# Performance work log

Hardware: AMD Instinct MI355X
Metric: run time of the kernel (lower is better)

## Reference

```python
import jax, jax.numpy as jnp
import numpy as np

B, C, H = 8, 768, 12
TH = TW = 16
SH = SW = 32
N = TH * TW + SH * SW  # 1280


def setup_inputs() -> dict:
    key = jax.random.key(0)
    k1, k2, k3 = jax.random.split(key, 3)
    return {
        "x": jax.random.normal(k1, (B, N, C), jnp.float32),
        "qkv_w": jax.random.normal(k2, (3 * C, C), jnp.float32) * 0.02,
        "proj_w": jax.random.normal(k3, (C, C), jnp.float32) * 0.02,
        "proj_b": jnp.zeros((C,), jnp.float32),
        "t_h": TH, "t_w": TW, "s_h": SH, "s_w": SW,
    }


def reference(x, qkv_w, proj_w, proj_b, t_h, t_w, s_h, s_w):
    Bb, Nn, Cc = x.shape
    hd = Cc // H
    scale = hd ** -0.5
    nt = t_h * t_w
    ns = s_h * s_w
    # qkv projection: torch Linear computes x @ W.T
    qkv = (x @ qkv_w.T).reshape(Bb, Nn, 3, H, hd).transpose(2, 0, 3, 1, 4)
    q, k, v = qkv[0], qkv[1], qkv[2]  # each [B, H, N, hd]
    q_mt, q_s = q[:, :, :nt], q[:, :, nt:]
    k_mt, v_mt = k[:, :, :nt], v[:, :, :nt]
    # template queries attend only to template keys
    attn_t = jax.nn.softmax(jnp.einsum('bhqd,bhkd->bhqk', q_mt, k_mt) * scale, axis=-1)
    x_mt = jnp.einsum('bhqk,bhkd->bhqd', attn_t, v_mt).transpose(0, 2, 1, 3).reshape(Bb, nt, Cc)
    # search queries attend to all (template + search) keys
    attn_s = jax.nn.softmax(jnp.einsum('bhqd,bhkd->bhqk', q_s, k) * scale, axis=-1)
    x_s = jnp.einsum('bhqk,bhkd->bhqd', attn_s, v).transpose(0, 2, 1, 3).reshape(Bb, ns, Cc)
    out = jnp.concatenate([x_mt, x_s], axis=1)
    out = out @ proj_w.T + proj_b
    return out
```

## Files before the change

kernel.cpp:

```cpp
#include <hip/hip_runtime.h>
#include <hip/hip_bf16.h>


typedef __attribute__((ext_vector_type(8))) short s8v;
typedef __attribute__((ext_vector_type(4))) float f4v;
typedef __attribute__((ext_vector_type(4))) unsigned short u4v;
typedef __attribute__((ext_vector_type(4))) unsigned int u4i;
typedef __attribute__((ext_vector_type(2))) unsigned int u2i;

#define MFMA16(a, b, c) __builtin_amdgcn_mfma_f32_16x16x32_bf16((a), (b), (c), 0, 0, 0)

#define QSCALE 0.1803368801f

__device__ __forceinline__ unsigned short f2bf(float f) {
  unsigned int u = __builtin_bit_cast(unsigned int, f);
  u += 0x7fffu + ((u >> 16) & 1u);
  return (unsigned short)(u >> 16);
}

__device__ __forceinline__ unsigned int pk2(float lo, float hi) {
  __hip_bfloat162 t = __float22bfloat162_rn(make_float2(lo, hi));
  unsigned int u;
  __builtin_memcpy(&u, &t, 4);
  return u;
}

__device__ __forceinline__ s8v pack8(const float* p0, const float* p1) {
  u4i pi;
  pi[0] = pk2(p0[0], p0[1]);
  pi[1] = pk2(p0[2], p0[3]);
  pi[2] = pk2(p1[0], p1[1]);
  pi[3] = pk2(p1[2], p1[3]);
  return __builtin_bit_cast(s8v, pi);
}

__global__ __launch_bounds__(256) void cvt3_kernel(const float* __restrict__ x,
                                                   const float* __restrict__ wq,
                                                   const float* __restrict__ wp,
                                                   unsigned short* __restrict__ xb,
                                                   unsigned short* __restrict__ wqb,
                                                   unsigned short* __restrict__ wpb) {
  int i = blockIdx.x * 256 + threadIdx.x;
  const float* src;
  unsigned short* dst;
  int j;
  if (i < 1966080) {
    src = x; dst = xb; j = i;
  } else if (i < 1966080 + 442368) {
    src = wq; dst = wqb; j = i - 1966080;
  } else {
    src = wp; dst = wpb; j = i - (1966080 + 442368);
  }
  f4v v = ((const f4v*)src)[j];
  u4v o;
  o[0] = f2bf(v[0]); o[1] = f2bf(v[1]); o[2] = f2bf(v[2]); o[3] = f2bf(v[3]);
  ((u4v*)dst)[j] = o;
}


#define GEMM_STAGE(AS, BS, kt_)                                                             \
  do {                                                                                      \
    __builtin_amdgcn_global_load_lds(                                                       \
        (const __attribute__((address_space(1))) unsigned int*)(gA0 + (kt_)),               \
        (__attribute__((address_space(3))) unsigned int*)((char*)(AS) + tid * 16), 16, 0, 0); \
    __builtin_amdgcn_global_load_lds(                                                       \
        (const __attribute__((address_space(1))) unsigned int*)(gB0 + (kt_)),               \
        (__attribute__((address_space(3))) unsigned int*)((char*)(BS) + tid * 16), 16, 0, 0); \
    __builtin_amdgcn_global_load_lds(                                                       \
        (const __attribute__((address_space(1))) unsigned int*)(gA1 + (kt_)),               \
        (__attribute__((address_space(3))) unsigned int*)((char*)(AS) + (256 + tid) * 16),  \
        16, 0, 0);                                                                          \
    __builtin_amdgcn_global_load_lds(                                                       \
        (const __attribute__((address_space(1))) unsigned int*)(gB1 + (kt_)),               \
        (__attribute__((address_space(3))) unsigned int*)((char*)(BS) + (256 + tid) * 16),  \
        16, 0, 0);                                                                          \
  } while (0)

__global__ __launch_bounds__(256) void gemm_qkv_kernel(
    const unsigned short* __restrict__ A,
    const unsigned short* __restrict__ Bm,
    unsigned short* __restrict__ qb, unsigned short* __restrict__ kb,
    unsigned short* __restrict__ vT) {
  const int K = 768;
  __shared__ __align__(16) unsigned short As[2][128 * 32];
  __shared__ __align__(16) unsigned short Bs[2][128 * 32];
  int tid = threadIdx.x;
  int wave = tid >> 6, lane = tid & 63;
  int quad = lane >> 4, l16 = lane & 15;
  int wm = wave >> 1, wn = wave & 1;
  int m0 = blockIdx.y * 128, n0 = blockIdx.x * 128;

  int srow = tid >> 2, scol = (tid & 3) << 3;
  const unsigned short* gA0 = A + (size_t)(m0 + srow) * K + scol;
  const unsigned short* gA1 = A + (size_t)(m0 + srow + 64) * K + scol;
  const unsigned short* gB0 = Bm + (size_t)(n0 + srow) * K + scol;
  const unsigned short* gB1 = Bm + (size_t)(n0 + srow + 64) * K + scol;

  f4v acc[4][4];
#pragma unroll
  for (int i = 0; i < 4; ++i)
#pragma unroll
    for (int j = 0; j < 4; ++j) acc[i][j] = (f4v){0.f, 0.f, 0.f, 0.f};

  GEMM_STAGE(As[0], Bs[0], 0);

  for (int t = 0; t < 24; ++t) {
    __syncthreads();
    int bf = t & 1;
    if (t + 1 < 24) GEMM_STAGE(As[bf ^ 1], Bs[bf ^ 1], (t + 1) * 32);

    const unsigned short* Ab = As[bf];
    const unsigned short* Bb = Bs[bf];
    s8v af[4], bfr[4];
#pragma unroll
    for (int mi = 0; mi < 4; ++mi)
      af[mi] = *(const s8v*)&Ab[(wm * 64 + mi * 16 + l16) * 32 + quad * 8];
#pragma unroll
    for (int ni = 0; ni < 4; ++ni)
      bfr[ni] = *(const s8v*)&Bb[(wn * 64 + ni * 16 + l16) * 32 + quad * 8];
#pragma unroll
    for (int mi = 0; mi < 4; ++mi)
#pragma unroll
      for (int ni = 0; ni < 4; ++ni)
        acc[mi][ni] = MFMA16(af[mi], bfr[ni], acc[mi][ni]);
  }

  int which = n0 / 768;
  if (which == 2) {
#pragma unroll
    for (int ni = 0; ni < 4; ++ni) {
      int oo = n0 + wn * 64 + ni * 16 + l16 - 1536;
      int hh = oo >> 6;
      int dd = oo & 63;
#pragma unroll
      for (int mi = 0; mi < 4; ++mi) {
        int gm = m0 + wm * 64 + mi * 16 + quad * 4;
        int bb = gm / 1280;
        int nn = gm - bb * 1280;
        u2i w;
        w[0] = pk2(acc[mi][ni][0], acc[mi][ni][1]);
        w[1] = pk2(acc[mi][ni][2], acc[mi][ni][3]);
        *(u2i*)(vT + (((size_t)bb * 12 + hh) * 64 + dd) * 1280 + nn) = w;
      }
    }
  } else {
    unsigned short* dst = which ? kb : qb;
    float sc = which ? 1.0f : QSCALE;
#pragma unroll
    for (int ni = 0; ni < 4; ++ni) {
      int oo = n0 + wn * 64 + ni * 16 + l16 - which * 768;
      int hh = oo >> 6;
      int dd = oo & 63;
#pragma unroll
      for (int mi = 0; mi < 4; ++mi) {
#pragma unroll
        for (int r = 0; r < 4; ++r) {
          int gm = m0 + wm * 64 + mi * 16 + quad * 4 + r;
          int bb = gm / 1280;
          int nn = gm - bb * 1280;
          dst[(((size_t)bb * 12 + hh) * 1280 + nn) * 64 + dd] = f2bf(acc[mi][ni][r] * sc);
        }
      }
    }
  }
}

__global__ __launch_bounds__(256) void gemm_proj_kernel(
    const unsigned short* __restrict__ A,
    const unsigned short* __restrict__ Bm,
    const float* __restrict__ pb, float* __restrict__ out) {
  const int K = 768;
  __shared__ __align__(16) unsigned short As[2][128 * 32];
  __shared__ __align__(16) unsigned short Bs[2][128 * 32];
  int tid = threadIdx.x;
  int wave = tid >> 6, lane = tid & 63;
  int quad = lane >> 4, l16 = lane & 15;
  int wm = wave >> 1, wn = wave & 1;
  int m0 = blockIdx.y * 128, n0 = blockIdx.x * 128;

  int srow = tid >> 2, scol = (tid & 3) << 3;
  const unsigned short* gA0 = A + (size_t)(m0 + srow) * K + scol;
  const unsigned short* gA1 = A + (size_t)(m0 + srow + 64) * K + scol;
  const unsigned short* gB0 = Bm + (size_t)(n0 + srow) * K + scol;
  const unsigned short* gB1 = Bm + (size_t)(n0 + srow + 64) * K + scol;

  f4v acc[4][4];
#pragma unroll
  for (int i = 0; i < 4; ++i)
#pragma unroll
    for (int j = 0; j < 4; ++j) acc[i][j] = (f4v){0.f, 0.f, 0.f, 0.f};

  GEMM_STAGE(As[0], Bs[0], 0);

  for (int t = 0; t < 24; ++t) {
    __syncthreads();
    int bf = t & 1;
    if (t + 1 < 24) GEMM_STAGE(As[bf ^ 1], Bs[bf ^ 1], (t + 1) * 32);

    const unsigned short* Ab = As[bf];
    const unsigned short* Bb = Bs[bf];
    s8v af[4], bfr[4];
#pragma unroll
    for (int mi = 0; mi < 4; ++mi)
      af[mi] = *(const s8v*)&Ab[(wm * 64 + mi * 16 + l16) * 32 + quad * 8];
#pragma unroll
    for (int ni = 0; ni < 4; ++ni)
      bfr[ni] = *(const s8v*)&Bb[(wn * 64 + ni * 16 + l16) * 32 + quad * 8];
#pragma unroll
    for (int mi = 0; mi < 4; ++mi)
#pragma unroll
      for (int ni = 0; ni < 4; ++ni)
        acc[mi][ni] = MFMA16(af[mi], bfr[ni], acc[mi][ni]);
  }

#pragma unroll
  for (int ni = 0; ni < 4; ++ni) {
    int gn = n0 + wn * 64 + ni * 16 + l16;
    float bias = pb[gn];
#pragma unroll
    for (int mi = 0; mi < 4; ++mi)
#pragma unroll
      for (int r = 0; r < 4; ++r) {
        int gm = m0 + wm * 64 + mi * 16 + quad * 4 + r;
        out[(size_t)gm * 768 + gn] = acc[mi][ni][r] + bias;
      }
  }
}

__global__ __launch_bounds__(256) void attn_kernel(
    const unsigned short* __restrict__ qb, const unsigned short* __restrict__ kb,
    const unsigned short* __restrict__ vT, unsigned short* __restrict__ attnb) {
  const int NT = 1280, CC = 768;
  int bx = blockIdx.x;
  int h = blockIdx.y;
  int b = blockIdx.z;
  int nk, qstart;
  if (bx < 8) { nk = 1280; qstart = 256 + bx * 128; }
  else        { nk = 256;  qstart = (bx - 8) * 128; }
  int wave = threadIdx.x >> 6, lane = threadIdx.x & 63;
  int quad = lane >> 4, l16 = lane & 15;
  int qa = qstart + wave * 32;
  int ntiles = nk >> 6;

  const unsigned short* qp = qb + (((size_t)b * 12 + h) * NT + qa) * 64;
  const unsigned short* kp = kb + (((size_t)b * 12 + h) * NT) * 64;
  const unsigned short* vp = vT + (((size_t)b * 12 + h) * 64) * NT;

  __shared__ __align__(16) unsigned short Kl[2][8][512];
  __shared__ __align__(16) unsigned short Vl[2][8][512];

  s8v bq0 = *(const s8v*)(qp + l16 * 64 + quad * 8);
  s8v bq1 = *(const s8v*)(qp + l16 * 64 + 32 + quad * 8);
  s8v bq2 = *(const s8v*)(qp + (16 + l16) * 64 + quad * 8);
  s8v bq3 = *(const s8v*)(qp + (16 + l16) * 64 + 32 + quad * 8);

  int perm = ((l16 >> 2) << 3) + (l16 & 3);
  int f0 = wave * 2, f1 = wave * 2 + 1;
  int koffs0, koffs1, voffs0, voffs1;
  {
    int s = f0 >> 2, dh = (f0 >> 1) & 1, hh = f0 & 1;
    koffs0 = (s * 32 + hh * 4 + perm) * 64 + (dh * 4 + quad) * 8;
    s = f1 >> 2; dh = (f1 >> 1) & 1; hh = f1 & 1;
    koffs1 = (s * 32 + hh * 4 + perm) * 64 + (dh * 4 + quad) * 8;
    int dt = f0 >> 1, sv = f0 & 1;
    voffs0 = (dt * 16 + l16) * NT + sv * 32 + quad * 8;
    dt = f1 >> 1; sv = f1 & 1;
    voffs1 = (dt * 16 + l16) * NT + sv * 32 + quad * 8;
  }

#define STAGE(bfi, k0_)                                                                     \
  do {                                                                                      \
    __builtin_amdgcn_global_load_lds(                                                       \
        (const __attribute__((address_space(1))) unsigned int*)(kp + (size_t)(k0_)*64 +     \
                                                                koffs0),                    \
        (__attribute__((address_space(3))) unsigned int*)((char*)&Kl[bfi][f0][0] +          \
                                                          lane * 16),                       \
        16, 0, 0);                                                                          \
    __builtin_amdgcn_global_load_lds(                                                       \
        (const __attribute__((address_space(1))) unsigned int*)(kp + (size_t)(k0_)*64 +     \
                                                                koffs1),                    \
        (__attribute__((address_space(3))) unsigned int*)((char*)&Kl[bfi][f1][0] +          \
                                                          lane * 16),                       \
        16, 0, 0);                                                                          \
    __builtin_amdgcn_global_load_lds(                                                       \
        (const __attribute__((address_space(1))) unsigned int*)(vp + (size_t)(k0_) +        \
                                                                voffs0),                    \
        (__attribute__((address_space(3))) unsigned int*)((char*)&Vl[bfi][f0][0] +          \
                                                          lane * 16),                       \
        16, 0, 0);                                                                          \
    __builtin_amdgcn_global_load_lds(                                                       \
        (const __attribute__((address_space(1))) unsigned int*)(vp + (size_t)(k0_) +        \
                                                                voffs1),                    \
        (__attribute__((address_space(3))) unsigned int*)((char*)&Vl[bfi][f1][0] +          \
                                                          lane * 16),                       \
        16, 0, 0);                                                                          \
  } while (0)

  float la = 0.f, lb = 0.f;
  f4v Oa[4], Ob[4];
#pragma unroll
  for (int dt = 0; dt < 4; ++dt) {
    Oa[dt] = (f4v){0.f, 0.f, 0.f, 0.f};
    Ob[dt] = (f4v){0.f, 0.f, 0.f, 0.f};
  }

  STAGE(0, 0);

  for (int t = 0; t < ntiles; ++t) {
    __syncthreads();
    int bf = t & 1;
    if (t + 1 < ntiles) STAGE(bf ^ 1, (t + 1) * 64);

    s8v kf[8], vf[8];
#pragma unroll
    for (int f = 0; f < 8; ++f) kf[f] = *(const s8v*)&Kl[bf][f][lane * 8];
#pragma unroll
    for (int g = 0; g < 8; ++g) vf[g] = *(const s8v*)&Vl[bf][g][lane * 8];

#pragma unroll
    for (int s = 0; s < 2; ++s) {
      int s4 = s << 2;
      f4v s0a = {0.f, 0.f, 0.f, 0.f}, s1a = {0.f, 0.f, 0.f, 0.f};
      f4v s0b = {0.f, 0.f, 0.f, 0.f}, s1b = {0.f, 0.f, 0.f, 0.f};
      s0a = MFMA16(kf[s4 | 0], bq0, s0a);
      s0a = MFMA16(kf[s4 | 2], bq1, s0a);
      s1a = MFMA16(kf[s4 | 1], bq0, s1a);
      s1a = MFMA16(kf[s4 | 3], bq1, s1a);
      s0b = MFMA16(kf[s4 | 0], bq2, s0b);
      s0b = MFMA16(kf[s4 | 2], bq3, s0b);
      s1b = MFMA16(kf[s4 | 1], bq2, s1b);
      s1b = MFMA16(kf[s4 | 3], bq3, s1b);

      float p0a[4], p1a[4], p0b[4], p1b[4];
#pragma unroll
      for (int r = 0; r < 4; ++r) {
        p0a[r] = __builtin_amdgcn_exp2f(s0a[r]);
        p1a[r] = __builtin_amdgcn_exp2f(s1a[r]);
        p0b[r] = __builtin_amdgcn_exp2f(s0b[r]);
        p1b[r] = __builtin_amdgcn_exp2f(s1b[r]);
      }
      la += ((p0a[0] + p0a[1]) + (p0a[2] + p0a[3])) + ((p1a[0] + p1a[1]) + (p1a[2] + p1a[3]));
      lb += ((p0b[0] + p0b[1]) + (p0b[2] + p0b[3])) + ((p1b[0] + p1b[1]) + (p1b[2] + p1b[3]));

      s8v pa = pack8(p0a, p1a);
      s8v pbv = pack8(p0b, p1b);

#pragma unroll
      for (int dt = 0; dt < 4; ++dt) {
        Oa[dt] = MFMA16(vf[dt * 2 + s], pa, Oa[dt]);
        Ob[dt] = MFMA16(vf[dt * 2 + s], pbv, Ob[dt]);
      }
    }
  }
#undef STAGE

  la += __shfl_xor(la, 16, 64);
  la += __shfl_xor(la, 32, 64);
  lb += __shfl_xor(lb, 16, 64);
  lb += __shfl_xor(lb, 32, 64);
  float inva = 1.f / la, invb = 1.f / lb;

  size_t rowa = ((size_t)b * NT + qa + l16) * CC + h * 64;
  size_t rowb = ((size_t)b * NT + qa + 16 + l16) * CC + h * 64;
#pragma unroll
  for (int dt = 0; dt < 4; ++dt) {
    u4v ova, ovb;
#pragma unroll
    for (int r = 0; r < 4; ++r) {
      ova[r] = f2bf(Oa[dt][r] * inva);
      ovb[r] = f2bf(Ob[dt][r] * invb);
    }
    *(u4v*)(attnb + rowa + dt * 16 + quad * 4) = ova;
    *(u4v*)(attnb + rowb + dt * 16 + quad * 4) = ovb;
  }
}

extern "C" void kernel_launch(void* const* d_in, const int* in_sizes, int n_in,
                              void* d_out, int out_size, void* d_ws, size_t ws_size,
                              hipStream_t stream) {
  const float* x = (const float*)d_in[0];
  const float* qkv_w = (const float*)d_in[1];
  const float* proj_w = (const float*)d_in[2];
  const float* proj_b = (const float*)d_in[3];
  float* out = (float*)d_out;

  char* ws = (char*)d_ws;
  unsigned short* xb = (unsigned short*)(ws + 0);
  unsigned short* wqkvb = (unsigned short*)(ws + 15728640);
  unsigned short* wpb = (unsigned short*)(ws + 19267584);
  unsigned short* qb = (unsigned short*)(ws + 20447232);
  unsigned short* kbuf = (unsigned short*)(ws + 36175872);
  unsigned short* vT = (unsigned short*)(ws + 51904512);
  unsigned short* attnb = xb;

  cvt3_kernel<<<dim3(9984), 256, 0, stream>>>(x, qkv_w, proj_w, xb, wqkvb, wpb);

  gemm_qkv_kernel<<<dim3(18, 80), 256, 0, stream>>>(xb, wqkvb, qb, kbuf, vT);
  attn_kernel<<<dim3(10, 12, 8), 256, 0, stream>>>(qb, kbuf, vT, attnb);
  gemm_proj_kernel<<<dim3(6, 80), 256, 0, stream>>>(attnb, wpb, proj_b, out);
}
```

Measured before the change: 272.0 us.

## Triple-buffer LDS loads with vmcnt waits and remap blocks per XCD

All three GEMM/attention kernels move from double to triple buffering in LDS. Two tiles are kept in flight, and each step waits with explicit s_waitcnt vmcnt(4) plus a raw s_barrier instead of __syncthreads. The grids are also flattened to 1D and remapped so consecutive blocks on the same XCD share rows or batch-heads, aiming for better L2 locality. The extra buffer raises LDS use, which may reduce occupancy. The hand-counted vmcnt value depends on each stage issuing exactly four loads per thread, which holds for the GEMMs but is less certain for the attention STAGE.

Result: faster. 242.0 us (-11.0%).

```diff
diff --git a/kernel.cpp b/kernel.cpp
--- a/kernel.cpp
+++ b/kernel.cpp
@@ -76,19 +76,32 @@
         16, 0, 0);                                                                          \
   } while (0)
 
+#define PIPE_WAIT(cond_more)                                                                \
+  do {                                                                                      \
+    if (cond_more) asm volatile("s_waitcnt vmcnt(4) lgkmcnt(0)" ::: "memory");              \
+    else           asm volatile("s_waitcnt vmcnt(0) lgkmcnt(0)" ::: "memory");              \
+    __builtin_amdgcn_s_barrier();                                                           \
+    __builtin_amdgcn_sched_barrier(0);                                                      \
+  } while (0)
+
 __global__ __launch_bounds__(256) void gemm_qkv_kernel(
     const unsigned short* __restrict__ A,
     const unsigned short* __restrict__ Bm,
     unsigned short* __restrict__ qb, unsigned short* __restrict__ kb,
     unsigned short* __restrict__ vT) {
   const int K = 768;
-  __shared__ __align__(16) unsigned short As[2][128 * 32];
-  __shared__ __align__(16) unsigned short Bs[2][128 * 32];
+  __shared__ __align__(16) unsigned short As[3][128 * 32];
+  __shared__ __align__(16) unsigned short Bs[3][128 * 32];
   int tid = threadIdx.x;
   int wave = tid >> 6, lane = tid & 63;
   int quad = lane >> 4, l16 = lane & 15;
   int wm = wave >> 1, wn = wave & 1;
-  int m0 = blockIdx.y * 128, n0 = blockIdx.x * 128;
+  int l = blockIdx.x;
+  int xcd = l & 7;
+  int idx = l >> 3;
+  int by = xcd * 10 + idx / 18;
+  int bxg = idx - (idx / 18) * 18;
+  int m0 = by * 128, n0 = bxg * 128;
 
   int srow = tid >> 2, scol = (tid & 3) << 3;
   const unsigned short* gA0 = A + (size_t)(m0 + srow) * K + scol;
@@ -103,14 +116,15 @@
     for (int j = 0; j < 4; ++j) acc[i][j] = (f4v){0.f, 0.f, 0.f, 0.f};
 
   GEMM_STAGE(As[0], Bs[0], 0);
-
+  GEMM_STAGE(As[1], Bs[1], 32);
+
+  int bfc = 0, bfs = 2;
   for (int t = 0; t < 24; ++t) {
-    __syncthreads();
-    int bf = t & 1;
-    if (t + 1 < 24) GEMM_STAGE(As[bf ^ 1], Bs[bf ^ 1], (t + 1) * 32);
-
-    const unsigned short* Ab = As[bf];
-    const unsigned short* Bb = Bs[bf];
+    PIPE_WAIT(t + 1 < 24);
+    if (t + 2 < 24) GEMM_STAGE(As[bfs], Bs[bfs], (t + 2) * 32);
+
+    const unsigned short* Ab = As[bfc];
+    const unsigned short* Bb = Bs[bfc];
     s8v af[4], bfr[4];
 #pragma unroll
     for (int mi = 0; mi < 4; ++mi)
@@ -123,6 +137,9 @@
 #pragma unroll
       for (int ni = 0; ni < 4; ++ni)
         acc[mi][ni] = MFMA16(af[mi], bfr[ni], acc[mi][ni]);
+
+    bfc = (bfc == 2) ? 0 : bfc + 1;
+    bfs = (bfs == 2) ? 0 : bfs + 1;
   }
 
   int which = n0 / 768;
@@ -170,13 +187,18 @@
     const unsigned short* __restrict__ Bm,
     const float* __restrict__ pb, float* __restrict__ out) {
   const int K = 768;
-  __shared__ __align__(16) unsigned short As[2][128 * 32];
-  __shared__ __align__(16) unsigned short Bs[2][128 * 32];
+  __shared__ __align__(16) unsigned short As[3][128 * 32];
+  __shared__ __align__(16) unsigned short Bs[3][128 * 32];
   int tid = threadIdx.x;
   int wave = tid >> 6, lane = tid & 63;
   int quad = lane >> 4, l16 = lane & 15;
   int wm = wave >> 1, wn = wave & 1;
-  int m0 = blockIdx.y * 128, n0 = blockIdx.x * 128;
+  int l = blockIdx.x;
+  int xcd = l & 7;
+  int idx = l >> 3;
+  int by = xcd * 10 + idx / 6;
+  int bxg = idx - (idx / 6) * 6;
+  int m0 = by * 128, n0 = bxg * 128;
 
   int srow = tid >> 2, scol = (tid & 3) << 3;
   const unsigned short* gA0 = A + (size_t)(m0 + srow) * K + scol;
@@ -191,14 +213,15 @@
     for (int j = 0; j < 4; ++j) acc[i][j] = (f4v){0.f, 0.f, 0.f, 0.f};
 
   GEMM_STAGE(As[0], Bs[0], 0);
-
+  GEMM_STAGE(As[1], Bs[1], 32);
+
+  int bfc = 0, bfs = 2;
   for (int t = 0; t < 24; ++t) {
-    __syncthreads();
-    int bf = t & 1;
-    if (t + 1 < 24) GEMM_STAGE(As[bf ^ 1], Bs[bf ^ 1], (t + 1) * 32);
-
-    const unsigned short* Ab = As[bf];
-    const unsigned short* Bb = Bs[bf];
+    PIPE_WAIT(t + 1 < 24);
+    if (t + 2 < 24) GEMM_STAGE(As[bfs], Bs[bfs], (t + 2) * 32);
+
+    const unsigned short* Ab = As[bfc];
+    const unsigned short* Bb = Bs[bfc];
     s8v af[4], bfr[4];
 #pragma unroll
     for (int mi = 0; mi < 4; ++mi)
@@ -211,6 +234,9 @@
 #pragma unroll
       for (int ni = 0; ni < 4; ++ni)
         acc[mi][ni] = MFMA16(af[mi], bfr[ni], acc[mi][ni]);
+
+    bfc = (bfc == 2) ? 0 : bfc + 1;
+    bfs = (bfs == 2) ? 0 : bfs + 1;
   }
 
 #pragma unroll
@@ -231,9 +257,13 @@
     const unsigned short* __restrict__ qb, const unsigned short* __restrict__ kb,
     const unsigned short* __restrict__ vT, unsigned short* __restrict__ attnb) {
   const int NT = 1280, CC = 768;
-  int bx = blockIdx.x;
-  int h = blockIdx.y;
-  int b = blockIdx.z;
+  int l = blockIdx.x;
+  int xcd = l & 7;
+  int idx = l >> 3;
+  int grp = xcd * 12 + idx / 10;
+  int bx = idx - (idx / 10) * 10;
+  int b = grp / 12;
+  int h = grp - b * 12;
   int nk, qstart;
   if (bx < 8) { nk = 1280; qstart = 256 + bx * 128; }
   else        { nk = 256;  qstart = (bx - 8) * 128; }
@@ -246,8 +276,8 @@
   const unsigned short* kp = kb + (((size_t)b * 12 + h) * NT) * 64;
   const unsigned short* vp = vT + (((size_t)b * 12 + h) * 64) * NT;
 
-  __shared__ __align__(16) unsigned short Kl[2][8][512];
-  __shared__ __align__(16) unsigned short Vl[2][8][512];
+  __shared__ __align__(16) unsigned short Kl[3][8][512];
+  __shared__ __align__(16) unsigned short Vl[3][8][512];
 
   s8v bq0 = *(const s8v*)(qp + l16 * 64 + quad * 8);
   s8v bq1 = *(const s8v*)(qp + l16 * 64 + 32 + quad * 8);
@@ -305,17 +335,18 @@
   }
 
   STAGE(0, 0);
-
+  STAGE(1, 64);
+
+  int bfc = 0, bfs = 2;
   for (int t = 0; t < ntiles; ++t) {
-    __syncthreads();
-    int bf = t & 1;
-    if (t + 1 < ntiles) STAGE(bf ^ 1, (t + 1) * 64);
+    PIPE_WAIT(t + 1 < ntiles);
+    if (t + 2 < ntiles) STAGE(bfs, (t + 2) * 64);
 
     s8v kf[8], vf[8];
 #pragma unroll
-    for (int f = 0; f < 8; ++f) kf[f] = *(const s8v*)&Kl[bf][f][lane * 8];
-#pragma unroll
-    for (int g = 0; g < 8; ++g) vf[g] = *(const s8v*)&Vl[bf][g][lane * 8];
+    for (int f = 0; f < 8; ++f) kf[f] = *(const s8v*)&Kl[bfc][f][lane * 8];
+#pragma unroll
+    for (int g = 0; g < 8; ++g) vf[g] = *(const s8v*)&Vl[bfc][g][lane * 8];
 
 #pragma unroll
     for (int s = 0; s < 2; ++s) {
@@ -351,6 +382,9 @@
         Ob[dt] = MFMA16(vf[dt * 2 + s], pbv, Ob[dt]);
       }
     }
+
+    bfc = (bfc == 2) ? 0 : bfc + 1;
+    bfs = (bfs == 2) ? 0 : bfs + 1;
   }
 #undef STAGE
 
@@ -395,7 +429,7 @@
 
   cvt3_kernel<<<dim3(9984), 256, 0, stream>>>(x, qkv_w, proj_w, xb, wqkvb, wpb);
 
-  gemm_qkv_kernel<<<dim3(18, 80), 256, 0, stream>>>(xb, wqkvb, qb, kbuf, vT);
-  attn_kernel<<<dim3(10, 12, 8), 256, 0, stream>>>(qb, kbuf, vT, attnb);
-  gemm_proj_kernel<<<dim3(6, 80), 256, 0, stream>>>(attnb, wpb, proj_b, out);
-}
+  gemm_qkv_kernel<<<dim3(1440), 256, 0, stream>>>(xb, wqkvb, qb, kbuf, vT);
+  attn_kernel<<<dim3(960), 256, 0, stream>>>(qb, kbuf, vT, attnb);
+  gemm_proj_kernel<<<dim3(480), 256, 0, stream>>>(attnb, wpb, proj_b, out);
+}
```

## Remap blocks to XCDs for L2 locality and add explicit drain barriers

Applied to the files above, without the earlier changes.

All three main kernels now launch 1D grids and remap block indices so that each XCD (blockIdx mod 8) handles a contiguous set of M-rows or batch/head groups. This keeps shared A/K/V data within one XCD's L2. The __syncthreads before each prefetch is replaced with an explicit waitcnt(0) plus barrier and sched_barrier. In attention, V fragments are loaded from LDS just before their MFMAs rather than up front, which lowers register pressure, and the MFMA bursts are wrapped in s_setprio. The full waitcnt drain and the sched_barrier may limit the compiler's overlap of loads and compute.

After: 257.5 us. 5.3% less time.

```diff
diff --git a/kernel.cpp b/kernel.cpp
--- a/kernel.cpp
+++ b/kernel.cpp
@@ -33,6 +33,13 @@
   pi[3] = pk2(p1[2], p1[3]);
   return __builtin_bit_cast(s8v, pi);
 }
+
+#define DRAIN_BAR                                                                           \
+  do {                                                                                      \
+    asm volatile("s_waitcnt vmcnt(0) lgkmcnt(0)" ::: "memory");                             \
+    __builtin_amdgcn_s_barrier();                                                           \
+    __builtin_amdgcn_sched_barrier(0);                                                      \
+  } while (0)
 
 __global__ __launch_bounds__(256) void cvt3_kernel(const float* __restrict__ x,
                                                    const float* __restrict__ wq,
@@ -88,7 +95,12 @@
   int wave = tid >> 6, lane = tid & 63;
   int quad = lane >> 4, l16 = lane & 15;
   int wm = wave >> 1, wn = wave & 1;
-  int m0 = blockIdx.y * 128, n0 = blockIdx.x * 128;
+  int l = blockIdx.x;
+  int xcd = l & 7;
+  int idx = l >> 3;
+  int by = xcd * 10 + idx / 18;
+  int bxg = idx - (idx / 18) * 18;
+  int m0 = by * 128, n0 = bxg * 128;
 
   int srow = tid >> 2, scol = (tid & 3) << 3;
   const unsigned short* gA0 = A + (size_t)(m0 + srow) * K + scol;
@@ -105,8 +117,8 @@
   GEMM_STAGE(As[0], Bs[0], 0);
 
   for (int t = 0; t < 24; ++t) {
-    __syncthreads();
     int bf = t & 1;
+    DRAIN_BAR;
     if (t + 1 < 24) GEMM_STAGE(As[bf ^ 1], Bs[bf ^ 1], (t + 1) * 32);
 
     const unsigned short* Ab = As[bf];
@@ -176,7 +188,12 @@
   int wave = tid >> 6, lane = tid & 63;
   int quad = lane >> 4, l16 = lane & 15;
   int wm = wave >> 1, wn = wave & 1;
-  int m0 = blockIdx.y * 128, n0 = blockIdx.x * 128;
+  int l = blockIdx.x;
+  int xcd = l & 7;
+  int idx = l >> 3;
+  int by = xcd * 10 + idx / 6;
+  int bxg = idx - (idx / 6) * 6;
+  int m0 = by * 128, n0 = bxg * 128;
 
   int srow = tid >> 2, scol = (tid & 3) << 3;
   const unsigned short* gA0 = A + (size_t)(m0 + srow) * K + scol;
@@ -193,8 +210,8 @@
   GEMM_STAGE(As[0], Bs[0], 0);
 
   for (int t = 0; t < 24; ++t) {
-    __syncthreads();
     int bf = t & 1;
+    DRAIN_BAR;
     if (t + 1 < 24) GEMM_STAGE(As[bf ^ 1], Bs[bf ^ 1], (t + 1) * 32);
 
     const unsigned short* Ab = As[bf];
@@ -231,9 +248,13 @@
     const unsigned short* __restrict__ qb, const unsigned short* __restrict__ kb,
     const unsigned short* __restrict__ vT, unsigned short* __restrict__ attnb) {
   const int NT = 1280, CC = 768;
-  int bx = blockIdx.x;
-  int h = blockIdx.y;
-  int b = blockIdx.z;
+  int l = blockIdx.x;
+  int xcd = l & 7;
+  int idx = l >> 3;
+  int grp = xcd * 12 + idx / 10;
+  int bx = idx - (idx / 10) * 10;
+  int b = grp / 12;
+  int h = grp - b * 12;
   int nk, qstart;
   if (bx < 8) { nk = 1280; qstart = 256 + bx * 128; }
   else        { nk = 256;  qstart = (bx - 8) * 128; }
@@ -307,21 +328,20 @@
   STAGE(0, 0);
 
   for (int t = 0; t < ntiles; ++t) {
-    __syncthreads();
     int bf = t & 1;
+    DRAIN_BAR;
     if (t + 1 < ntiles) STAGE(bf ^ 1, (t + 1) * 64);
 
-    s8v kf[8], vf[8];
-#pragma unroll
-    for (int f = 0; f < 8; ++f) kf[f] = *(const s8v*)&Kl[bf][f][lane * 8];
-#pragma unroll
-    for (int g = 0; g < 8; ++g) vf[g] = *(const s8v*)&Vl[bf][g][lane * 8];
+    s8v kf[8];
+#pragma unroll
+    for (int ff = 0; ff < 8; ++ff) kf[ff] = *(const s8v*)&Kl[bf][ff][lane * 8];
 
 #pragma unroll
     for (int s = 0; s < 2; ++s) {
       int s4 = s << 2;
       f4v s0a = {0.f, 0.f, 0.f, 0.f}, s1a = {0.f, 0.f, 0.f, 0.f};
       f4v s0b = {0.f, 0.f, 0.f, 0.f}, s1b = {0.f, 0.f, 0.f, 0.f};
+      __builtin_amdgcn_s_setprio(1);
       s0a = MFMA16(kf[s4 | 0], bq0, s0a);
       s0a = MFMA16(kf[s4 | 2], bq1, s0a);
       s1a = MFMA16(kf[s4 | 1], bq0, s1a);
@@ -330,6 +350,7 @@
       s0b = MFMA16(kf[s4 | 2], bq3, s0b);
       s1b = MFMA16(kf[s4 | 1], bq2, s1b);
       s1b = MFMA16(kf[s4 | 3], bq3, s1b);
+      __builtin_amdgcn_s_setprio(0);
 
       float p0a[4], p1a[4], p0b[4], p1b[4];
 #pragma unroll
@@ -345,11 +366,16 @@
       s8v pa = pack8(p0a, p1a);
       s8v pbv = pack8(p0b, p1b);
 
+      s8v vf[4];
+#pragma unroll
+      for (int dt = 0; dt < 4; ++dt) vf[dt] = *(const s8v*)&Vl[bf][dt * 2 + s][lane * 8];
+      __builtin_amdgcn_s_setprio(1);
 #pragma unroll
       for (int dt = 0; dt < 4; ++dt) {
-        Oa[dt] = MFMA16(vf[dt * 2 + s], pa, Oa[dt]);
-        Ob[dt] = MFMA16(vf[dt * 2 + s], pbv, Ob[dt]);
+        Oa[dt] = MFMA16(vf[dt], pa, Oa[dt]);
+        Ob[dt] = MFMA16(vf[dt], pbv, Ob[dt]);
       }
+      __builtin_amdgcn_s_setprio(0);
     }
   }
 #undef STAGE
@@ -395,7 +421,7 @@
 
   cvt3_kernel<<<dim3(9984), 256, 0, stream>>>(x, qkv_w, proj_w, xb, wqkvb, wpb);
 
-  gemm_qkv_kernel<<<dim3(18, 80), 256, 0, stream>>>(xb, wqkvb, qb, kbuf, vT);
-  attn_kernel<<<dim3(10, 12, 8), 256, 0, stream>>>(qb, kbuf, vT, attnb);
-  gemm_proj_kernel<<<dim3(6, 80), 256, 0, stream>>>(attnb, wpb, proj_b, out);
-}
+  gemm_qkv_kernel<<<dim3(1440), 256, 0, stream>>>(xb, wqkvb, qb, kbuf, vT);
+  attn_kernel<<<dim3(960), 256, 0, stream>>>(qb, kbuf, vT, attnb);
+  gemm_proj_kernel<<<dim3(480), 256, 0, stream>>>(attnb, wpb, proj_b, out);
+}
```
